# Optimization experiments

Measured on AMD Instinct MI355X. Metric: run time of the kernel, lower is better.

Reference implementation:

```python
import jax, jax.numpy as jnp
import numpy as np

N_HEADS = 16
N_QUBITS = 7
DIM = 2 ** N_QUBITS  # per-head state dimension = 128


def _rotation_gates(params):
    """params: [H, nq, 3] -> composite Rz@Ry@Rx gates [H, nq, 2, 2] complex64."""
    a = params[..., 0] / 2.0
    b = params[..., 1] / 2.0
    c = params[..., 2] / 2.0
    ca, sa = jnp.cos(a), jnp.sin(a)
    cb, sb = jnp.cos(b), jnp.sin(b)
    i_ = jnp.complex64(1j)
    rx = jnp.stack([jnp.stack([ca + 0j, -i_ * sa], -1),
                    jnp.stack([-i_ * sa, ca + 0j], -1)], -2)  # [H,nq,2,2]
    ry = jnp.stack([jnp.stack([cb + 0j, -sb + 0j], -1),
                    jnp.stack([sb + 0j, cb + 0j], -1)], -2)
    z = jnp.zeros_like(c) + 0j
    rz = jnp.stack([jnp.stack([jnp.exp(-i_ * c), z], -1),
                    jnp.stack([z, jnp.exp(i_ * c)], -1)], -2)
    return jnp.einsum('...ij,...jk,...kl->...il', rz, ry, rx).astype(jnp.complex64)


def _quantum_transform(states, params):
    """states: [B,S,H,D] real; params: [H,nq,3]. Apply per-qubit gates then measure |psi|^2.
    Qubit q acts on axis q of the state reshaped to [2]*n_qubits (q=0 most significant)."""
    B, S, H, D = states.shape
    gates = _rotation_gates(params)  # [H, nq, 2, 2]
    psi = states.astype(jnp.complex64)
    for q in range(N_QUBITS):
        L = 2 ** q
        R = D // (2 * L)
        psi = psi.reshape(B, S, H, L, 2, R)
        psi = jnp.einsum('hij,bshljr->bshlir', gates[:, q], psi)
        psi = psi.reshape(B, S, H, D)
    return psi.real ** 2 + psi.imag ** 2  # measurement probabilities, real fp32


def setup_inputs() -> dict:
    key = jax.random.key(0)
    ks = jax.random.split(key, 6)
    B, S = 2, 2048
    return {
        'states': jax.random.normal(ks[0], (B, S, N_HEADS * DIM), dtype=jnp.float32),
        'attention_mask': jnp.ones((B, S), dtype=jnp.int32),
        'query_params': jax.random.normal(ks[1], (N_HEADS, N_QUBITS, 3), dtype=jnp.float32),
        'key_params': jax.random.normal(ks[2], (N_HEADS, N_QUBITS, 3), dtype=jnp.float32),
        'value_params': jax.random.normal(ks[3], (N_HEADS, N_QUBITS, 3), dtype=jnp.float32),
        'W_out': jax.random.normal(ks[4], (DIM, N_HEADS * DIM), dtype=jnp.float32) / np.sqrt(N_HEADS * DIM),
        'b_out': jnp.zeros((DIM,), dtype=jnp.float32),
    }


def reference(states, attention_mask, query_params, key_params, value_params, W_out, b_out):
    B, S, F = states.shape
    x = states.reshape(B, S, N_HEADS, DIM)  # split heads
    q = _quantum_transform(x, query_params)   # [B,S,H,D]
    k = _quantum_transform(x, key_params)
    v = _quantum_transform(x, value_params)
    scores = jnp.einsum('bqhd,bkhd->bhqk', q, k) / np.sqrt(DIM)  # [B,H,S,S]
    mask = attention_mask[:, None, None, :] != 0  # [B,1,1,S]
    scores = jnp.where(mask, scores, jnp.float32(-jnp.inf))
    probs = jax.nn.softmax(scores, axis=-1)
    ctx = jnp.einsum('bhqk,bkhd->bqhd', probs, v)  # [B,S,H,D]
    concat = ctx.reshape(B, S, N_HEADS * DIM)
    return concat @ W_out.T + b_out  # [B,S,D]
```

## Files before the change

kernel.cpp:

```cpp
#include <hip/hip_runtime.h>
#include <math.h>

#define NH 16
#define DD 128
#define SS 2048
#define NQ 7

typedef __attribute__((ext_vector_type(8))) short bf16x8;
typedef __attribute__((ext_vector_type(16))) float f32x16;

#define MFMA32(a,b,c) __builtin_amdgcn_mfma_f32_32x32x16_bf16(a,b,c,0,0,0)

__device__ __forceinline__ unsigned pkbf(float a, float b){
    unsigned ua = __float_as_uint(a); ua += 0x7FFF + ((ua>>16)&1);
    unsigned ub = __float_as_uint(b); ub += 0x7FFF + ((ub>>16)&1);
    return (ua>>16) | (ub & 0xFFFF0000u);
}

__device__ __forceinline__ void gl_lds16(const int4* g, int4* l){
    __builtin_amdgcn_global_load_lds((const __attribute__((address_space(1))) void*)g,
                                     (__attribute__((address_space(3))) void*)l, 16, 0, 0);
}

struct cplx { float r, i; };
__device__ __forceinline__ cplx cmul(cplx a, cplx b){ cplx o; o.r = a.r*b.r - a.i*b.i; o.i = a.r*b.i + a.i*b.r; return o; }
__device__ __forceinline__ cplx cadd(cplx a, cplx b){ cplx o; o.r = a.r+b.r; o.i = a.i+b.i; return o; }

__global__ void gates_kernel(const float* __restrict__ qp, const float* __restrict__ kp,
                             const float* __restrict__ vp, float* __restrict__ gates){
    for (int it = threadIdx.x; it < 3*NH*NQ; it += 256){
        int set = it / (NH*NQ);
        int rem = it % (NH*NQ);
        const float* p = (set==0 ? qp : (set==1 ? kp : vp)) + rem*3;
        float a = p[0]*0.5f, b = p[1]*0.5f, c = p[2]*0.5f;
        float ca=cosf(a), sa=sinf(a), cb=cosf(b), sb=sinf(b), cc=cosf(c), sc=sinf(c);
        cplx rx00={ca,0.f}, rx01={0.f,-sa}, rx10={0.f,-sa}, rx11={ca,0.f};
        cplx ry00={cb,0.f}, ry01={-sb,0.f}, ry10={sb,0.f}, ry11={cb,0.f};
        cplx e0={cc,-sc}, e1={cc,sc};
        cplx m00 = cadd(cmul(ry00,rx00), cmul(ry01,rx10));
        cplx m01 = cadd(cmul(ry00,rx01), cmul(ry01,rx11));
        cplx m10 = cadd(cmul(ry10,rx00), cmul(ry11,rx10));
        cplx m11 = cadd(cmul(ry10,rx01), cmul(ry11,rx11));
        cplx g00 = cmul(e0,m00), g01 = cmul(e0,m01), g10 = cmul(e1,m10), g11 = cmul(e1,m11);
        float* gp = gates + it*8;
        gp[0]=g00.r; gp[1]=g00.i; gp[2]=g01.r; gp[3]=g01.i;
        gp[4]=g10.r; gp[5]=g10.i; gp[6]=g11.r; gp[7]=g11.i;
    }
}

__global__ __launch_bounds__(256) void prep2_kernel(const float* __restrict__ W,
        const float* __restrict__ gates, ushort* __restrict__ wfrag, ushort* __restrict__ ufrag){
    int t = threadIdx.x;
    if (blockIdx.x < 128){
        int tid = blockIdx.x*256 + t;
        int ln = tid & 31, hi = (tid>>5)&1, ds = (tid>>6)&127, ct = tid>>13;
        int n = ct*32 + ln;
        const float* src = W + (size_t)n*2048 + ds*16 + hi*8;
        float4 f0 = *(const float4*)(src);
        float4 f1 = *(const float4*)(src + 4);
        int4 o;
        o.x = (int)pkbf(f0.x, f0.y); o.y = (int)pkbf(f0.z, f0.w);
        o.z = (int)pkbf(f1.x, f1.y); o.w = (int)pkbf(f1.z, f1.w);
        ((int4*)wfrag)[tid] = o;
        return;
    }
    int sh = blockIdx.x - 128;
    const float* gp = gates + sh*NQ*8;
    float g[7][8];
    #pragma unroll
    for (int q=0;q<7;++q)
        #pragma unroll
        for (int e=0;e<8;++e) g[q][e] = gp[q*8+e];
    int4* uf = (int4*)ufrag;
    #pragma unroll
    for (int p=0;p<8;++p){
        int pos = t + p*256;
        int ln = pos & 31, hi = (pos>>5)&1, ds = (pos>>6)&7, ct = pos>>9;
        int dp = ct*32 + ln;
        int d0 = ds*16 + hi*8;
        cplx base = {1.f, 0.f};
        #pragma unroll
        for (int q=0;q<4;++q){
            int rb = (dp >> (6-q)) & 1, cb2 = (d0 >> (6-q)) & 1;
            cplx gv = { g[q][rb*4+cb2*2], g[q][rb*4+cb2*2+1] };
            base = cmul(base, gv);
        }
        int r4 = (dp>>2)&1, r5 = (dp>>1)&1, r6 = dp&1;
        float vr[8], vi[8];
        #pragma unroll
        for (int j=0;j<8;++j){
            cplx g4 = { g[4][r4*4 + ((j>>2)&1)*2], g[4][r4*4 + ((j>>2)&1)*2 + 1] };
            cplx g5 = { g[5][r5*4 + ((j>>1)&1)*2], g[5][r5*4 + ((j>>1)&1)*2 + 1] };
            cplx g6 = { g[6][r6*4 + (j&1)*2],      g[6][r6*4 + (j&1)*2 + 1] };
            cplx v = cmul(cmul(cmul(base, g4), g5), g6);
            vr[j] = v.r; vi[j] = v.i;
        }
        int4 outr, outi;
        outr.x = (int)pkbf(vr[0],vr[1]); outr.y = (int)pkbf(vr[2],vr[3]);
        outr.z = (int)pkbf(vr[4],vr[5]); outr.w = (int)pkbf(vr[6],vr[7]);
        outi.x = (int)pkbf(vi[0],vi[1]); outi.y = (int)pkbf(vi[2],vi[3]);
        outi.z = (int)pkbf(vi[4],vi[5]); outi.w = (int)pkbf(vi[6],vi[7]);
        uf[ ((sh*8 + ct)*8 + ds)*64 + hi*32 + ln ]     = outr;
        uf[ ((sh*8 + 4 + ct)*8 + ds)*64 + hi*32 + ln ] = outi;
    }
}

__global__ __launch_bounds__(256, 2) void qkv_kernel(const float* __restrict__ states,
        const ushort* __restrict__ ufrag, ushort* __restrict__ qfo,
        ushort* __restrict__ kfo, ushort* __restrict__ vfo){
    __shared__ int xs[128*66];
    int t = threadIdx.x, w = t>>6, lane = t&63, hi = lane>>5, ln = lane&31;
    int bh = blockIdx.x >> 4, stile = blockIdx.x & 15;
    int b = bh >> 4, h = bh & 15;
    int mt = stile*4 + w;
    const float sc = 0.08838834764831845f;
    {
        int tk = t >> 1, hf = t & 1;
        const float* src = states + ((size_t)(b*SS + stile*128 + tk))*2048 + h*128 + hf*64;
        int* dst = xs + tk*66 + hf*32;
        #pragma unroll
        for (int i=0;i<16;++i){
            float4 f = *(const float4*)(src + i*4);
            dst[i*2]   = (int)pkbf(f.x, f.y);
            dst[i*2+1] = (int)pkbf(f.z, f.w);
        }
    }
    __syncthreads();
    bf16x8 xf[8];
    #pragma unroll
    for (int ds=0; ds<8; ++ds){
        union { bf16x8 v; int2 d[2]; } c;
        const int2* base = (const int2*)(xs + (w*32 + ln)*66 + ds*8 + hi*4);
        c.d[0] = base[0]; c.d[1] = base[1];
        xf[ds] = c.v;
    }
    const int4* ub = (const int4*)ufrag;
    int4* qf4 = (int4*)qfo; int4* kf4 = (int4*)kfo; int4* vf4 = (int4*)vfo;
    #pragma unroll
    for (int set=0; set<3; ++set){
        int sh = set*16 + h;
        #pragma unroll
        for (int ct=0; ct<4; ++ct){
            bf16x8 ur[8], ui[8];
            #pragma unroll
            for (int ds=0; ds<8; ++ds){
                ur[ds] = *(const bf16x8*)(ub + ((sh*8 + ct)*8 + ds)*64 + lane);
                ui[ds] = *(const bf16x8*)(ub + ((sh*8 + 4 + ct)*8 + ds)*64 + lane);
            }
            f32x16 Cr, Ci;
            #pragma unroll
            for (int r=0;r<16;++r){ Cr[r]=0.f; Ci[r]=0.f; }
            if (set < 2){
                #pragma unroll
                for (int ds=0; ds<8; ++ds){
                    Cr = MFMA32(ur[ds], xf[ds], Cr);
                    Ci = MFMA32(ui[ds], xf[ds], Ci);
                }
            } else {
                #pragma unroll
                for (int ds=0; ds<8; ++ds){
                    Cr = MFMA32(xf[ds], ur[ds], Cr);
                    Ci = MFMA32(xf[ds], ui[ds], Ci);
                }
            }
            float pv[16];
            #pragma unroll
            for (int r=0;r<16;++r) pv[r] = Cr[r]*Cr[r] + Ci[r]*Ci[r];
            if (set == 0){
                #pragma unroll
                for (int r=0;r<16;++r) pv[r] *= sc;
            }
            unsigned u2[4][2];
            #pragma unroll
            for (int g2=0; g2<4; ++g2){
                u2[g2][0] = pkbf(pv[g2*4+0], pv[g2*4+1]);
                u2[g2][1] = pkbf(pv[g2*4+2], pv[g2*4+3]);
            }
            #pragma unroll
            for (int gg=0; gg<2; ++gg){
                int g2s = hi*2 + gg, g2p = g2s ^ 2;
                unsigned r0 = (unsigned)__shfl_xor((int)u2[g2p][0], 32);
                unsigned r1 = (unsigned)__shfl_xor((int)u2[g2p][1], 32);
                int4 frag;
                frag.x = (int)(hi ? r0 : u2[g2s][0]);
                frag.y = (int)(hi ? r1 : u2[g2s][1]);
                frag.z = (int)(hi ? u2[g2s][0] : r0);
                frag.w = (int)(hi ? u2[g2s][1] : r1);
                if (set == 0)
                    qf4[((bh*64 + mt)*8 + ct*2 + hi)*64 + gg*32 + ln] = frag;
                else if (set == 1)
                    kf4[((bh*64 + mt)*8 + ct*2 + hi)*64 + gg*32 + ln] = frag;
                else
                    vf4[((bh*4 + ct)*128 + mt*2 + hi)*64 + gg*32 + ln] = frag;
            }
        }
    }
}

__global__ __launch_bounds__(256, 2) void flash_kernel(const ushort* __restrict__ qfi,
        const ushort* __restrict__ kfi, const ushort* __restrict__ vfi,
        const int* __restrict__ mask, ushort* __restrict__ ctxf){
    __shared__ __align__(16) int4 kbuf[2][1024];
    __shared__ __align__(16) int4 vbuf[2][1024];
    int t = threadIdx.x, w = t>>6, lane = t&63, hi = lane>>5, ln = lane&31;
    int bh = blockIdx.x >> 4, qt = blockIdx.x & 15;
    int b = bh >> 4;
    const int4* qfp = (const int4*)qfi + (size_t)((bh*64 + qt*4 + w)*8)*64 + lane;
    bf16x8 qf[8];
    #pragma unroll
    for (int ds=0; ds<8; ++ds) qf[ds] = *(const bf16x8*)(qfp + ds*64);
    const int4* kg = (const int4*)kfi + (size_t)(bh*64*8)*64 + (w*4)*64 + lane;
    const int4* vg = (const int4*)vfi + ((size_t)(bh*4 + w)*128)*64 + lane;
    const int* mp = mask + b*SS;
    f32x16 O[4];
    #pragma unroll
    for (int d=0; d<4; ++d){
        #pragma unroll
        for (int r=0;r<16;++r) O[d][r] = 0.f;
    }
    float l = 0.f;
    {
        int4* kd = &kbuf[0][(w*4)*64];
        int4* vd = &vbuf[0][(w*4)*64];
        #pragma unroll
        for (int i=0;i<4;++i) gl_lds16(kg + i*64, kd + i*64);
        #pragma unroll
        for (int i=0;i<4;++i) gl_lds16(vg + i*64, vd + i*64);
    }
    for (int kt=0; kt<32; ++kt){
        int p = kt & 1;
        int mk = mp[kt*64 + lane];
        __syncthreads();
        if (kt < 31){
            int4* kd = &kbuf[p^1][(w*4)*64];
            int4* vd = &vbuf[p^1][(w*4)*64];
            const int4* ks = kg + (size_t)(kt+1)*1024;
            const int4* vs = vg + (kt+1)*4*64;
            #pragma unroll
            for (int i=0;i<4;++i) gl_lds16(ks + i*64, kd + i*64);
            #pragma unroll
            for (int i=0;i<4;++i) gl_lds16(vs + i*64, vd + i*64);
        }
        const int4* kl = kbuf[p];
        const int4* vl = vbuf[p];
        f32x16 S0, S1;
        #pragma unroll
        for (int r=0;r<16;++r){ S0[r]=0.f; S1[r]=0.f; }
        #pragma unroll
        for (int ds=0; ds<8; ++ds){
            bf16x8 k0 = *(const bf16x8*)(kl + ds*64 + lane);
            bf16x8 k1 = *(const bf16x8*)(kl + (8+ds)*64 + lane);
            S0 = MFMA32(k0, qf[ds], S0);
            S1 = MFMA32(k1, qf[ds], S1);
        }
        if (__ballot(mk != 0) != ~0ull){
            #pragma unroll
            for (int r=0;r<16;++r){
                int row0 = ((r>>2)<<3) + (hi<<2) + (r&3);
                if (__shfl(mk, row0) == 0)      S0[r] = -1e30f;
                if (__shfl(mk, 32 + row0) == 0) S1[r] = -1e30f;
            }
        }
        #pragma unroll
        for (int r=0;r<16;++r){
            S0[r] = __expf(S0[r] - 40.f); l += S0[r];
            S1[r] = __expf(S1[r] - 40.f); l += S1[r];
        }
        #pragma unroll
        for (int m2=0; m2<2; ++m2){
            #pragma unroll
            for (int T=0; T<2; ++T){
                const f32x16& P = m2 ? S1 : S0;
                unsigned A0 = pkbf(P[8*T+0], P[8*T+1]);
                unsigned A1 = pkbf(P[8*T+2], P[8*T+3]);
                unsigned B0 = pkbf(P[8*T+4], P[8*T+5]);
                unsigned B1 = pkbf(P[8*T+6], P[8*T+7]);
                unsigned X0 = hi ? A0 : B0, X1 = hi ? A1 : B1;
                unsigned Y0 = (unsigned)__shfl_xor((int)X0, 32);
                unsigned Y1 = (unsigned)__shfl_xor((int)X1, 32);
                union { bf16x8 v; unsigned u[4]; } pf;
                pf.u[0] = hi ? Y0 : A0;
                pf.u[1] = hi ? Y1 : A1;
                pf.u[2] = hi ? B0 : Y0;
                pf.u[3] = hi ? B1 : Y1;
                int tt = m2*2 + T;
                #pragma unroll
                for (int db=0; db<4; ++db){
                    bf16x8 vf = *(const bf16x8*)(vl + (db*4 + tt)*64 + lane);
                    O[db] = MFMA32(vf, pf.v, O[db]);
                }
            }
        }
    }
    l += __shfl_xor(l, 32);
    float inv = 1.f / l;
    int h = bh & 15;
    int mt = b*64 + qt*4 + w;
    int4* cf = (int4*)ctxf;
    #pragma unroll
    for (int db=0; db<4; ++db){
        unsigned u[4][2];
        #pragma unroll
        for (int g2=0; g2<4; ++g2){
            u[g2][0] = pkbf(O[db][g2*4+0]*inv, O[db][g2*4+1]*inv);
            u[g2][1] = pkbf(O[db][g2*4+2]*inv, O[db][g2*4+3]*inv);
        }
        #pragma unroll
        for (int gg=0; gg<2; ++gg){
            int g2s = hi*2 + gg;
            int g2p = g2s ^ 2;
            unsigned r0 = (unsigned)__shfl_xor((int)u[g2p][0], 32);
            unsigned r1 = (unsigned)__shfl_xor((int)u[g2p][1], 32);
            int4 frag;
            frag.x = (int)(hi ? r0 : u[g2s][0]);
            frag.y = (int)(hi ? r1 : u[g2s][1]);
            frag.z = (int)(hi ? u[g2s][0] : r0);
            frag.w = (int)(hi ? u[g2s][1] : r1);
            int ds = h*8 + db*2 + hi;
            cf[ ((size_t)(mt*128 + ds)*2 + gg)*32 + ln ] = frag;
        }
    }
}

__global__ __launch_bounds__(256) void proj_kernel(const ushort* __restrict__ ctxf,
                                                   const ushort* __restrict__ wfrag,
                                                   const float* __restrict__ bo,
                                                   float* __restrict__ out){
    int t = threadIdx.x, w = t >> 6, lane = t & 63;
    int hi = lane >> 5, ln = lane & 31;
    int mt = blockIdx.x, ct = w;
    const int4* A = (const int4*)ctxf + (size_t)mt*8192 + lane;
    const int4* B = (const int4*)wfrag + (size_t)ct*8192 + lane;
    f32x16 acc;
    #pragma unroll
    for (int r=0;r<16;++r) acc[r] = 0.f;
    #pragma unroll 8
    for (int ds=0; ds<128; ++ds){
        bf16x8 a = *(const bf16x8*)(A + (size_t)ds*64);
        bf16x8 b = *(const bf16x8*)(B + (size_t)ds*64);
        acc = MFMA32(a, b, acc);
    }
    float bias = bo[ct*32 + ln];
    float* op = out + (size_t)(mt*32)*128 + ct*32 + ln;
    #pragma unroll
    for (int r=0;r<16;++r){
        int row = (r&3) + 8*(r>>2) + 4*hi;
        op[(size_t)row*128] = acc[r] + bias;
    }
}

extern "C" void kernel_launch(void* const* d_in, const int* in_sizes, int n_in,
                              void* d_out, int out_size, void* d_ws, size_t ws_size,
                              hipStream_t stream){
    const float* states = (const float*)d_in[0];
    const int*   mask   = (const int*)d_in[1];
    const float* qp     = (const float*)d_in[2];
    const float* kp     = (const float*)d_in[3];
    const float* vp     = (const float*)d_in[4];
    const float* W      = (const float*)d_in[5];
    const float* bo     = (const float*)d_in[6];
    float* out = (float*)d_out;
    char* wsb = (char*)d_ws;
    float*  gates = (float*) wsb;
    ushort* wfrag = (ushort*)(wsb + 16384);
    ushort* ufrag = (ushort*)(wsb + 16384 + 524288);
    char*   big   = wsb + 16384 + 524288 + 3145728;
    ushort* qf    = (ushort*)(big);
    ushort* kf    = (ushort*)(big + 1u*16777216);
    ushort* vf    = (ushort*)(big + 2u*16777216);
    ushort* ctxf  = (ushort*)(big + 3u*16777216);
    hipLaunchKernelGGL(gates_kernel, dim3(1), dim3(256), 0, stream, qp, kp, vp, gates);
    hipLaunchKernelGGL(prep2_kernel, dim3(176), dim3(256), 0, stream, W, gates, wfrag, ufrag);
    hipLaunchKernelGGL(qkv_kernel, dim3(512), dim3(256), 0, stream, states, ufrag, qf, kf, vf);
    hipLaunchKernelGGL(flash_kernel, dim3(512), dim3(256), 0, stream, qf, kf, vf, mask, ctxf);
    hipLaunchKernelGGL(proj_kernel, dim3(128), dim3(256), 0, stream, ctxf, wfrag, bo, out);
}
```

Before: 232.3 us.

## Split QKV kernel across sets, fold softmax offset into MFMA init with exp2

```diff
diff --git a/kernel.cpp b/kernel.cpp
--- a/kernel.cpp
+++ b/kernel.cpp
@@ -12,9 +12,14 @@
 #define MFMA32(a,b,c) __builtin_amdgcn_mfma_f32_32x32x16_bf16(a,b,c,0,0,0)
 
 __device__ __forceinline__ unsigned pkbf(float a, float b){
+#if __has_builtin(__builtin_amdgcn_cvt_pk_bf16_f32)
+    auto v = __builtin_amdgcn_cvt_pk_bf16_f32(a, b);
+    unsigned u; __builtin_memcpy(&u, &v, 4); return u;
+#else
     unsigned ua = __float_as_uint(a); ua += 0x7FFF + ((ua>>16)&1);
     unsigned ub = __float_as_uint(b); ub += 0x7FFF + ((ub>>16)&1);
     return (ua>>16) | (ub & 0xFFFF0000u);
+#endif
 }
 
 __device__ __forceinline__ void gl_lds16(const int4* g, int4* l){
@@ -105,94 +110,95 @@
     }
 }
 
-__global__ __launch_bounds__(256, 2) void qkv_kernel(const float* __restrict__ states,
+__global__ __launch_bounds__(256) void qkv_kernel(const float* __restrict__ states,
         const ushort* __restrict__ ufrag, ushort* __restrict__ qfo,
         ushort* __restrict__ kfo, ushort* __restrict__ vfo){
     __shared__ int xs[128*66];
     int t = threadIdx.x, w = t>>6, lane = t&63, hi = lane>>5, ln = lane&31;
-    int bh = blockIdx.x >> 4, stile = blockIdx.x & 15;
+    int blk = blockIdx.x;
+    int set = blk >> 9;
+    int r9  = blk & 511;
+    int bh = r9 >> 4, stile = r9 & 15;
     int b = bh >> 4, h = bh & 15;
-    int mt = stile*4 + w;
-    const float sc = 0.08838834764831845f;
+    const float sc = 0.12751743f;
     {
-        int tk = t >> 1, hf = t & 1;
-        const float* src = states + ((size_t)(b*SS + stile*128 + tk))*2048 + h*128 + hf*64;
-        int* dst = xs + tk*66 + hf*32;
+        int c = t & 31, tk2 = t >> 5;
         #pragma unroll
         for (int i=0;i<16;++i){
-            float4 f = *(const float4*)(src + i*4);
-            dst[i*2]   = (int)pkbf(f.x, f.y);
-            dst[i*2+1] = (int)pkbf(f.z, f.w);
+            int tk = i*8 + tk2;
+            const float* src = states + ((size_t)(b*SS + stile*128 + tk))*2048 + h*128 + c*4;
+            float4 f = *(const float4*)src;
+            int2 o; o.x = (int)pkbf(f.x,f.y); o.y = (int)pkbf(f.z,f.w);
+            *(int2*)(xs + tk*66 + c*2) = o;
         }
     }
     __syncthreads();
-    bf16x8 xf[8];
-    #pragma unroll
-    for (int ds=0; ds<8; ++ds){
-        union { bf16x8 v; int2 d[2]; } c;
-        const int2* base = (const int2*)(xs + (w*32 + ln)*66 + ds*8 + hi*4);
-        c.d[0] = base[0]; c.d[1] = base[1];
-        xf[ds] = c.v;
-    }
+    int ct = w;
+    int sh = set*16 + h;
     const int4* ub = (const int4*)ufrag;
     int4* qf4 = (int4*)qfo; int4* kf4 = (int4*)kfo; int4* vf4 = (int4*)vfo;
-    #pragma unroll
-    for (int set=0; set<3; ++set){
-        int sh = set*16 + h;
-        #pragma unroll
-        for (int ct=0; ct<4; ++ct){
-            bf16x8 ur[8], ui[8];
+    bf16x8 ur[8], ui[8];
+    #pragma unroll
+    for (int ds=0; ds<8; ++ds){
+        ur[ds] = *(const bf16x8*)(ub + ((sh*8 + ct)*8 + ds)*64 + lane);
+        ui[ds] = *(const bf16x8*)(ub + ((sh*8 + 4 + ct)*8 + ds)*64 + lane);
+    }
+    #pragma unroll 1
+    for (int tt=0; tt<4; ++tt){
+        bf16x8 xf[8];
+        #pragma unroll
+        for (int ds=0; ds<8; ++ds){
+            union { bf16x8 v; int2 d[2]; } c;
+            const int2* base = (const int2*)(xs + (tt*32 + ln)*66 + ds*8 + hi*4);
+            c.d[0] = base[0]; c.d[1] = base[1];
+            xf[ds] = c.v;
+        }
+        f32x16 Cr, Ci;
+        #pragma unroll
+        for (int r=0;r<16;++r){ Cr[r]=0.f; Ci[r]=0.f; }
+        if (set < 2){
             #pragma unroll
             for (int ds=0; ds<8; ++ds){
-                ur[ds] = *(const bf16x8*)(ub + ((sh*8 + ct)*8 + ds)*64 + lane);
-                ui[ds] = *(const bf16x8*)(ub + ((sh*8 + 4 + ct)*8 + ds)*64 + lane);
+                Cr = MFMA32(ur[ds], xf[ds], Cr);
+                Ci = MFMA32(ui[ds], xf[ds], Ci);
             }
-            f32x16 Cr, Ci;
-            #pragma unroll
-            for (int r=0;r<16;++r){ Cr[r]=0.f; Ci[r]=0.f; }
-            if (set < 2){
-                #pragma unroll
-                for (int ds=0; ds<8; ++ds){
-                    Cr = MFMA32(ur[ds], xf[ds], Cr);
-                    Ci = MFMA32(ui[ds], xf[ds], Ci);
-                }
-            } else {
-                #pragma unroll
-                for (int ds=0; ds<8; ++ds){
-                    Cr = MFMA32(xf[ds], ur[ds], Cr);
-                    Ci = MFMA32(xf[ds], ui[ds], Ci);
-                }
+        } else {
+            #pragma unroll
+            for (int ds=0; ds<8; ++ds){
+                Cr = MFMA32(xf[ds], ur[ds], Cr);
+                Ci = MFMA32(xf[ds], ui[ds], Ci);
             }
-            float pv[16];
-            #pragma unroll
-            for (int r=0;r<16;++r) pv[r] = Cr[r]*Cr[r] + Ci[r]*Ci[r];
-            if (set == 0){
-                #pragma unroll
-                for (int r=0;r<16;++r) pv[r] *= sc;
-            }
-            unsigned u2[4][2];
-            #pragma unroll
-            for (int g2=0; g2<4; ++g2){
-                u2[g2][0] = pkbf(pv[g2*4+0], pv[g2*4+1]);
-                u2[g2][1] = pkbf(pv[g2*4+2], pv[g2*4+3]);
-            }
-            #pragma unroll
-            for (int gg=0; gg<2; ++gg){
-                int g2s = hi*2 + gg, g2p = g2s ^ 2;
-                unsigned r0 = (unsigned)__shfl_xor((int)u2[g2p][0], 32);
-                unsigned r1 = (unsigned)__shfl_xor((int)u2[g2p][1], 32);
-                int4 frag;
-                frag.x = (int)(hi ? r0 : u2[g2s][0]);
-                frag.y = (int)(hi ? r1 : u2[g2s][1]);
-                frag.z = (int)(hi ? u2[g2s][0] : r0);
-                frag.w = (int)(hi ? u2[g2s][1] : r1);
-                if (set == 0)
-                    qf4[((bh*64 + mt)*8 + ct*2 + hi)*64 + gg*32 + ln] = frag;
-                else if (set == 1)
-                    kf4[((bh*64 + mt)*8 + ct*2 + hi)*64 + gg*32 + ln] = frag;
-                else
-                    vf4[((bh*4 + ct)*128 + mt*2 + hi)*64 + gg*32 + ln] = frag;
-            }
+        }
+        float pv[16];
+        #pragma unroll
+        for (int r=0;r<16;++r) pv[r] = Cr[r]*Cr[r] + Ci[r]*Ci[r];
+        if (set == 0){
+            #pragma unroll
+            for (int r=0;r<16;++r) pv[r] *= sc;
+        }
+        unsigned u2[4][2];
+        #pragma unroll
+        for (int g2=0; g2<4; ++g2){
+            u2[g2][0] = pkbf(pv[g2*4+0], pv[g2*4+1]);
+            u2[g2][1] = pkbf(pv[g2*4+2], pv[g2*4+3]);
+        }
+        int mt = stile*4 + tt;
+        #pragma unroll
+        for (int gg=0; gg<2; ++gg){
+            int g2s = hi*2 + gg, g2p = g2s ^ 2;
+            unsigned r0 = (unsigned)__shfl_xor((int)u2[g2p][0], 32);
+            unsigned r1 = (unsigned)__shfl_xor((int)u2[g2p][1], 32);
+            int4 frag;
+            frag.x = (int)(hi ? r0 : u2[g2s][0]);
+            frag.y = (int)(hi ? r1 : u2[g2s][1]);
+            frag.z = (int)(hi ? u2[g2s][0] : r0);
+            frag.w = (int)(hi ? u2[g2s][1] : r1);
+            if (set == 0)
+                qf4[((bh*64 + mt)*8 + ct*2 + hi)*64 + gg*32 + ln] = frag;
+            else if (set == 1)
+                kf4[((bh*64 + mt)*8 + ct*2 + hi)*64 + gg*32 + ln] = frag;
+            else
+                vf4[((bh*4 + ct)*128 + mt*2 + hi)*64 + gg*32 + ln] = frag;
         }
     }
 }
@@ -205,6 +211,7 @@
     int t = threadIdx.x, w = t>>6, lane = t&63, hi = lane>>5, ln = lane&31;
     int bh = blockIdx.x >> 4, qt = blockIdx.x & 15;
     int b = bh >> 4;
+    const float NEGC = -57.7078018f;
     const int4* qfp = (const int4*)qfi + (size_t)((bh*64 + qt*4 + w)*8)*64 + lane;
     bf16x8 qf[8];
     #pragma unroll
@@ -245,7 +252,7 @@
         const int4* vl = vbuf[p];
         f32x16 S0, S1;
         #pragma unroll
-        for (int r=0;r<16;++r){ S0[r]=0.f; S1[r]=0.f; }
+        for (int r=0;r<16;++r){ S0[r]=NEGC; S1[r]=NEGC; }
         #pragma unroll
         for (int ds=0; ds<8; ++ds){
             bf16x8 k0 = *(const bf16x8*)(kl + ds*64 + lane);
@@ -263,8 +270,8 @@
         }
         #pragma unroll
         for (int r=0;r<16;++r){
-            S0[r] = __expf(S0[r] - 40.f); l += S0[r];
-            S1[r] = __expf(S1[r] - 40.f); l += S1[r];
+            S0[r] = exp2f(S0[r]); l += S0[r];
+            S1[r] = exp2f(S1[r]); l += S1[r];
         }
         #pragma unroll
         for (int m2=0; m2<2; ++m2){
@@ -371,7 +378,7 @@
     ushort* ctxf  = (ushort*)(big + 3u*16777216);
     hipLaunchKernelGGL(gates_kernel, dim3(1), dim3(256), 0, stream, qp, kp, vp, gates);
     hipLaunchKernelGGL(prep2_kernel, dim3(176), dim3(256), 0, stream, W, gates, wfrag, ufrag);
-    hipLaunchKernelGGL(qkv_kernel, dim3(512), dim3(256), 0, stream, states, ufrag, qf, kf, vf);
+    hipLaunchKernelGGL(qkv_kernel, dim3(1536), dim3(256), 0, stream, states, ufrag, qf, kf, vf);
     hipLaunchKernelGGL(flash_kernel, dim3(512), dim3(256), 0, stream, qf, kf, vf, mask, ctxf);
     hipLaunchKernelGGL(proj_kernel, dim3(128), dim3(256), 0, stream, ctxf, wfrag, bo, out);
 }
```

New measurement: 251.4 us. 1.08x slower.
